# Optimization experiments

Hardware: AMD Instinct MI355X
Metric: run time of the kernel (lower is better)

## Reference

```python
import jax, jax.numpy as jnp
import numpy as np

B, L, C, H = 2, 2048, 1024, 16
D = C // H
THETA = 50000.0


def rotate_half(x):
    x1, x2 = jnp.split(x, 2, axis=-1)
    return jnp.concatenate((-x2, x1), axis=-1)


def rope_freqs(n, dim):
    inv_freq = 1.0 / (THETA ** (jnp.arange(0, dim, 2, dtype=jnp.float32) / dim))
    freqs = jnp.arange(n, dtype=jnp.float32)[:, None] * inv_freq[None, :]  # [n, dim//2]
    return jnp.concatenate((freqs, freqs), axis=-1)  # [n, dim]


def setup_inputs() -> dict:
    key = jax.random.key(0)
    ks = jax.random.split(key, 8)
    q = jax.random.normal(ks[0], (B, L, C), dtype=jnp.float32)
    mask = jax.random.randint(ks[1], (B, L), 0, 2) > 0
    mask = mask.at[:, 0].set(True)  # avoid fully-masked rows
    s = 1.0 / np.sqrt(C)
    Wq = jax.random.normal(ks[2], (C, C), dtype=jnp.float32) * s
    Wk = jax.random.normal(ks[3], (C, C), dtype=jnp.float32) * s
    Wv = jax.random.normal(ks[4], (C, C), dtype=jnp.float32) * s
    Wo = jax.random.normal(ks[5], (C, C), dtype=jnp.float32) * s
    bo = jnp.zeros((C,), dtype=jnp.float32)
    return {"q": q, "mask": mask, "Wq": Wq, "Wk": Wk, "Wv": Wv, "Wo": Wo, "bo": bo}


def reference(q, mask, Wq, Wk, Wv, Wo, bo):
    x = q
    # QKV projections (torch Linear: y = x @ W.T)
    def proj(W):
        y = jnp.einsum('blc,oc->blo', x, W)
        return y.reshape(B, L, H, D).transpose(0, 2, 1, 3)  # [B,H,L,D]
    qh, kh, vh = proj(Wq), proj(Wk), proj(Wv)
    # RoPE (L == S)
    pos = rope_freqs(L, D)  # [L, D]
    cos, sin = jnp.cos(pos), jnp.sin(pos)
    qh = qh * cos + rotate_half(qh) * sin
    kh = kh * cos + rotate_half(kh) * sin
    # masked SDPA with additive bias (-inf where mask is False)
    scale = 1.0 / np.sqrt(D)
    bias = jnp.where(mask[:, None, None, :], 0.0, -jnp.inf)  # [B,1,1,S]
    scores = jnp.einsum('bhld,bhsd->bhls', qh, kh) * scale + bias
    attn = jax.nn.softmax(scores, axis=-1)
    out = jnp.einsum('bhls,bhsd->bhld', attn, vh)
    out = out.transpose(0, 2, 1, 3).reshape(B, L, C)
    return jnp.einsum('blc,oc->blo', out, Wo) + bo
```

## Files before the change

### kernel.cpp

```cpp
#include <hip/hip_runtime.h>
#include <hip/hip_bf16.h>

typedef __hip_bfloat16 bf16;
typedef short bf16x8 __attribute__((ext_vector_type(8)));
typedef short bf16x4 __attribute__((ext_vector_type(4)));
typedef float floatx4 __attribute__((ext_vector_type(4)));

#define Bb 2
#define Ll 2048
#define Cc 1024
#define Hh 16
#define Dd 64
#define INVFREQ_LN 0.3381180763f
#define QSCALE 0.125f
#define NCONV 4096

#define GLD16(gp, lp) __builtin_amdgcn_global_load_lds( \
    (const __attribute__((address_space(1))) void*)(gp), \
    (__attribute__((address_space(3))) void*)(lp), 16, 0, 0)

__device__ inline short f2bf(float f) {
    __hip_bfloat16 h = __float2bfloat16(f);
    return *reinterpret_cast<short*>(&h);
}
__device__ inline short f2bf_rn(float f) {
    return (short)((__float_as_uint(f) + 0x8000u) >> 16);
}

__global__ __launch_bounds__(256) void convert_scan(
    const float* __restrict__ x, const float* __restrict__ wq,
    const float* __restrict__ wk, const float* __restrict__ wv,
    const float* __restrict__ wo,
    bf16* __restrict__ xb, bf16* __restrict__ wqkv, bf16* __restrict__ wob,
    const int* __restrict__ mask, int* __restrict__ cidx, int* __restrict__ valid)
{
    if (blockIdx.x >= NCONV) {
        const int b   = blockIdx.x - NCONV;
        const int tid = threadIdx.x;
        const int base = b * Ll + tid * 8;
        int m[8]; int s = 0;
        #pragma unroll
        for (int i = 0; i < 8; i++) { m[i] = mask[base + i] ? 1 : 0; s += m[i]; }
        const int lane = tid & 63;
        int xx = s;
        #pragma unroll
        for (int off = 1; off < 64; off <<= 1) {
            int y = __shfl_up(xx, off);
            if (lane >= off) xx += y;
        }
        __shared__ int wtot[4];
        if (lane == 63) wtot[tid >> 6] = xx;
        __syncthreads();
        int wbase = 0;
        const int w = tid >> 6;
        #pragma unroll
        for (int i = 0; i < 4; i++) if (i < w) wbase += wtot[i];
        int run = wbase + (xx - s);
        #pragma unroll
        for (int i = 0; i < 8; i++) { cidx[base + i] = run; run += m[i]; }
        if (tid == 255) valid[b] = run;
        return;
    }

    const int XN = (Bb * Ll * Cc) / 8;
    const int WN = (Cc * Cc) / 8;
    int i = blockIdx.x * 256 + threadIdx.x;
    const float* src; bf16* dst;
    if (i < XN)               { src = x  + (size_t)i * 8;                 dst = xb   + (size_t)i * 8; }
    else if (i < XN + WN)     { int j = i - XN;        src = wq + (size_t)j * 8; dst = wqkv + (size_t)j * 8; }
    else if (i < XN + 2*WN)   { int j = i - XN - WN;   src = wk + (size_t)j * 8; dst = wqkv + (size_t)Cc*Cc     + (size_t)j * 8; }
    else if (i < XN + 3*WN)   { int j = i - XN - 2*WN; src = wv + (size_t)j * 8; dst = wqkv + (size_t)Cc*Cc*2   + (size_t)j * 8; }
    else                      { int j = i - XN - 3*WN; src = wo + (size_t)j * 8; dst = wob  + (size_t)j * 8; }
    float4 a = *reinterpret_cast<const float4*>(src);
    float4 b = *reinterpret_cast<const float4*>(src + 4);
    float vv[8] = {a.x, a.y, a.z, a.w, b.x, b.y, b.z, b.w};
    bf16x8 o;
    #pragma unroll
    for (int t = 0; t < 8; t++) o[t] = f2bf(vv[t]);
    *reinterpret_cast<bf16x8*>(dst) = o;
}

template <int ROWS, int NTHREADS>
__device__ __forceinline__ void stage_swz(const bf16* __restrict__ g, int ldk,
                                          short* lds, int tid)
{
    #pragma unroll
    for (int s = 0; s < (ROWS * 4) / NTHREADS; s++) {
        const int idx = s * NTHREADS + tid;
        const int r   = idx >> 2;
        const int col = ((idx & 3) ^ ((r >> 1) & 3)) << 3;
        GLD16(g + (size_t)r * ldk + col, lds + idx * 8);
    }
}

#define VMCNT(N) asm volatile("s_waitcnt vmcnt(" #N ")" ::: "memory")

__global__ __launch_bounds__(512, 2) void gemm_qkv(
    const bf16* __restrict__ A, const bf16* __restrict__ W,
    bf16* __restrict__ qb, bf16* __restrict__ kb, bf16* __restrict__ vb,
    const int* __restrict__ cmask, const int* __restrict__ cidx)
{
    constexpr int K = Cc;
    constexpr int T = K / 32;

    __shared__ __align__(16) short As[3][256 * 32];
    __shared__ __align__(16) short Bs[3][256 * 32];

    const int tid  = threadIdx.x;
    const int wave = tid >> 6;
    const int lane = tid & 63;
    const int l15  = lane & 15;
    const int quad = lane >> 4;
    const int wm   = wave >> 2;
    const int wn   = wave & 3;

    const int lin = blockIdx.y * 12 + blockIdx.x;
    const int swz = (lin & 7) * 24 + (lin >> 3);
    const int m0  = (swz / 12) * 256;
    const int n0  = (swz % 12) * 256;

    const bf16* Ag = A + (size_t)m0 * K;
    const bf16* Wg = W + (size_t)n0 * K;

    const int gsw = (quad ^ ((l15 >> 1) & 3)) << 3;

    floatx4 acc[8][4];
    #pragma unroll
    for (int mt = 0; mt < 8; mt++)
        #pragma unroll
        for (int nt = 0; nt < 4; nt++)
            #pragma unroll
            for (int r = 0; r < 4; r++) acc[mt][nt][r] = 0.f;

    stage_swz<256, 512>(Ag,      K, &As[0][0], tid);
    stage_swz<256, 512>(Wg,      K, &Bs[0][0], tid);
    stage_swz<256, 512>(Ag + 32, K, &As[1][0], tid);
    stage_swz<256, 512>(Wg + 32, K, &Bs[1][0], tid);
    VMCNT(4);
    __builtin_amdgcn_s_barrier();

    int cur = 0;
    for (int t = 0; t < T; t++) {
        const short* Ac = &As[0][0] + cur * (256 * 32);
        const short* Bc = &Bs[0][0] + cur * (256 * 32);
        int nb = cur + 2; if (nb >= 3) nb -= 3;
        const int kk = (t + 2) << 5;

        bf16x8 bfr[4], af[4];
        #pragma unroll
        for (int nt = 0; nt < 4; nt++)
            bfr[nt] = *(const bf16x8*)(Bc + (wn * 64 + nt * 16 + l15) * 32 + gsw);
        #pragma unroll
        for (int mt = 0; mt < 4; mt++)
            af[mt] = *(const bf16x8*)(Ac + (wm * 128 + mt * 16 + l15) * 32 + gsw);
        if (t + 2 < T) stage_swz<256, 512>(Ag + kk, K, &As[nb][0], tid);
        __builtin_amdgcn_s_barrier();
        __builtin_amdgcn_s_setprio(1);
        #pragma unroll
        for (int mt = 0; mt < 4; mt++)
            #pragma unroll
            for (int nt = 0; nt < 4; nt++)
                acc[mt][nt] = __builtin_amdgcn_mfma_f32_16x16x32_bf16(
                    af[mt], bfr[nt], acc[mt][nt], 0, 0, 0);
        __builtin_amdgcn_s_setprio(0);
        __builtin_amdgcn_s_barrier();

        bf16x8 ag[4];
        #pragma unroll
        for (int mt = 0; mt < 4; mt++)
            ag[mt] = *(const bf16x8*)(Ac + (wm * 128 + (mt + 4) * 16 + l15) * 32 + gsw);
        if (t + 2 < T) stage_swz<256, 512>(Wg + kk, K, &Bs[nb][0], tid);
        __builtin_amdgcn_s_barrier();
        __builtin_amdgcn_s_setprio(1);
        #pragma unroll
        for (int mt = 0; mt < 4; mt++)
            #pragma unroll
            for (int nt = 0; nt < 4; nt++)
                acc[mt + 4][nt] = __builtin_amdgcn_mfma_f32_16x16x32_bf16(
                    ag[mt], bfr[nt], acc[mt + 4][nt], 0, 0, 0);
        __builtin_amdgcn_s_setprio(0);
        if (t + 2 < T) { VMCNT(4); }
        else           { VMCNT(0); }
        __builtin_amdgcn_s_barrier();

        cur++; if (cur == 3) cur = 0;
    }

    const int colbase = n0 + wn * 64;
    const int which   = colbase >> 10;
    const int hh      = (colbase & (Cc - 1)) >> 6;
    if (which == 2) {
        #pragma unroll
        for (int mt = 0; mt < 8; mt++)
            #pragma unroll
            for (int r = 0; r < 4; r++) {
                int row = m0 + wm * 128 + mt * 16 + quad * 4 + r;
                int b = row >> 11, l = row & (Ll - 1);
                if (cmask[b * Ll + l]) {
                    int c = cidx[b * Ll + l];
                    size_t head = (size_t)(b * Hh + hh) * Dd * Ll;
                    int lbase = (c & ~63) | (c & 7);
                    int lg    = (c >> 3) & 7;
                    #pragma unroll
                    for (int nt = 0; nt < 4; nt++) {
                        int d = nt * 16 + l15;
                        int pos = lbase | ((lg ^ (d & 7)) << 3);
                        vb[head + (size_t)d * Ll + pos] = __float2bfloat16(acc[mt][nt][r]);
                    }
                }
            }
    } else {
        bf16* dst = which ? kb : qb;
        const float qs = which ? 1.0f : QSCALE;
        const float base0 = __expf(-(float)l15 * INVFREQ_LN);
        const float base1 = __expf(-(float)(l15 + 16) * INVFREQ_LN);
        #pragma unroll
        for (int mt = 0; mt < 8; mt++)
            #pragma unroll
            for (int r = 0; r < 4; r++) {
                int row = m0 + wm * 128 + mt * 16 + quad * 4 + r;
                int b = row >> 11, l = row & (Ll - 1);
                int cm = 1, c = l;
                if (which == 1) {
                    cm = cmask[b * Ll + l];
                    c  = cidx[b * Ll + l];
                }
                if (cm) {
                    size_t rb = ((size_t)(b * Hh + hh) * Ll + c) * Dd;
                    #pragma unroll
                    for (int nt2 = 0; nt2 < 2; nt2++) {
                        float fr = (float)l * (nt2 ? base1 : base0);
                        float sn, cs;
                        __sincosf(fr, &sn, &cs);
                        float x1 = acc[mt][nt2][r];
                        float x2 = acc[mt][nt2 + 2][r];
                        float o1 = (x1 * cs - x2 * sn) * qs;
                        float o2 = (x2 * cs + x1 * sn) * qs;
                        int d1 = nt2 * 16 + l15;
                        int d2 = d1 + 32;
                        if (which == 1) {
                            int sw = c & 7;
                            int a1 = ((((d1 >> 3) ^ sw)) << 3) | (d1 & 7);
                            int a2 = ((((d2 >> 3) ^ sw)) << 3) | (d2 & 7);
                            dst[rb + a1] = __float2bfloat16(o1);
                            dst[rb + a2] = __float2bfloat16(o2);
                        } else {
                            dst[rb + d1] = __float2bfloat16(o1);
                            dst[rb + d2] = __float2bfloat16(o2);
                        }
                    }
                }
            }
    }
}

__global__ __launch_bounds__(256, 2) void gemm_out(
    const bf16* __restrict__ A, const bf16* __restrict__ W,
    float* __restrict__ outf, const float* __restrict__ bias)
{
    constexpr int K = Cc, N = Cc;
    constexpr int T = K / 32;

    __shared__ __align__(16) short As[3][64 * 32];
    __shared__ __align__(16) short Bs[3][128 * 32];

    const int tid  = threadIdx.x;
    const int wave = tid >> 6;
    const int lane = tid & 63;
    const int l15  = lane & 15;
    const int quad = lane >> 4;
    const int wm   = wave >> 1;
    const int wn   = wave & 1;

    const int lin = blockIdx.y * 8 + blockIdx.x;
    const int swz = (lin & 7) * 64 + (lin >> 3);
    const int m0  = (swz >> 3) * 64;
    const int n0  = (swz & 7) * 128;

    const bf16* Ag = A + (size_t)m0 * K;
    const bf16* Wg = W + (size_t)n0 * K;

    const int gsw = (quad ^ ((l15 >> 1) & 3)) << 3;

    floatx4 acc[2][4];
    #pragma unroll
    for (int mt = 0; mt < 2; mt++)
        #pragma unroll
        for (int nt = 0; nt < 4; nt++)
            #pragma unroll
            for (int r = 0; r < 4; r++) acc[mt][nt][r] = 0.f;

    stage_swz<64,  256>(Ag,      K, &As[0][0], tid);
    stage_swz<128, 256>(Wg,      K, &Bs[0][0], tid);
    stage_swz<64,  256>(Ag + 32, K, &As[1][0], tid);
    stage_swz<128, 256>(Wg + 32, K, &Bs[1][0], tid);
    VMCNT(3);
    __builtin_amdgcn_s_barrier();

    int cur = 0;
    for (int t = 0; t < T; t++) {
        const short* Ac = &As[0][0] + cur * (64 * 32);
        const short* Bc = &Bs[0][0] + cur * (128 * 32);

        if (t + 2 < T) {
            int nb = cur + 2; if (nb >= 3) nb -= 3;
            const int kk = (t + 2) << 5;
            stage_swz<64,  256>(Ag + kk, K, &As[nb][0], tid);
            stage_swz<128, 256>(Wg + kk, K, &Bs[nb][0], tid);
        }

        bf16x8 af[2], bfr[4];
        #pragma unroll
        for (int mt = 0; mt < 2; mt++)
            af[mt] = *(const bf16x8*)(Ac + (wm * 32 + mt * 16 + l15) * 32 + gsw);
        #pragma unroll
        for (int nt = 0; nt < 4; nt++)
            bfr[nt] = *(const bf16x8*)(Bc + (wn * 64 + nt * 16 + l15) * 32 + gsw);

        __builtin_amdgcn_s_setprio(1);
        #pragma unroll
        for (int mt = 0; mt < 2; mt++)
            #pragma unroll
            for (int nt = 0; nt < 4; nt++)
                acc[mt][nt] = __builtin_amdgcn_mfma_f32_16x16x32_bf16(
                    af[mt], bfr[nt], acc[mt][nt], 0, 0, 0);
        __builtin_amdgcn_s_setprio(0);

        if (t + 2 < T) { VMCNT(3); }
        else           { VMCNT(0); }
        __builtin_amdgcn_s_barrier();

        cur++; if (cur == 3) cur = 0;
    }

    #pragma unroll
    for (int mt = 0; mt < 2; mt++)
        #pragma unroll
        for (int r = 0; r < 4; r++) {
            int row = m0 + wm * 32 + mt * 16 + quad * 4 + r;
            #pragma unroll
            for (int nt = 0; nt < 4; nt++) {
                int col = n0 + wn * 64 + nt * 16 + l15;
                outf[(size_t)row * N + col] = acc[mt][nt][r] + bias[col];
            }
        }
}

#define LSTR 72

__global__ __launch_bounds__(512) void attn_mfma(
    const bf16* __restrict__ q, const bf16* __restrict__ k, const bf16* __restrict__ vt,
    const int* __restrict__ valid, bf16* __restrict__ ctx)
{
    __shared__ __align__(16) short Ks[2][64 * 64];
    __shared__ __align__(16) short Vs[2][64 * 64];
    __shared__ __align__(16) short Ps[8][16 * LSTR];

    const int tid  = threadIdx.x;
    const int wave = tid >> 6;
    const int lane = tid & 63;
    const int l15  = lane & 15;
    const int quad = lane >> 4;

    const int bh = blockIdx.x & 31;
    const int q0 = (blockIdx.x >> 5) << 7;
    const int b  = bh >> 4;
    const int h  = bh & (Hh - 1);

    const int nvalid = valid[b];
    const int ntiles = (nvalid + 63) >> 6;

    const short* qb  = (const short*)(q  + (size_t)bh * Ll * Dd);
    const short* kb  = (const short*)(k  + (size_t)bh * Ll * Dd);
    const short* vtb = (const short*)(vt + (size_t)bh * Dd * Ll);

    const int qrow = q0 + wave * 16 + l15;
    bf16x8 qa0 = *(const bf16x8*)(qb + (size_t)qrow * Dd + quad * 8);
    bf16x8 qa1 = *(const bf16x8*)(qb + (size_t)qrow * Dd + 32 + quad * 8);

    const int g0 = ((quad ^ (l15 & 7)) << 3);
    const int g1 = (((quad + 4) ^ (l15 & 7)) << 3);

    const short* vgp = vtb + (size_t)(tid >> 3) * Ll + ((tid & 7) << 3);
    short* ksl = &Ks[0][0] + tid * 8;
    short* vsl = &Vs[0][0] + tid * 8;
    const int lbuf = 64 * 64;

    floatx4 O[4];
    float l_r = 0.f;
    #pragma unroll
    for (int nt = 0; nt < 4; nt++)
        #pragma unroll
        for (int r = 0; r < 4; r++) O[nt][r] = 0.f;

    GLD16(kb + tid * 8, ksl);
    GLD16(vgp, vsl);

    for (int t = 0; t < ntiles; t++) {
        const int cur = t & 1;
        __syncthreads();
        if (t + 1 < ntiles) {
            const int s1 = (t + 1) << 6;
            GLD16(kb + (size_t)s1 * Dd + tid * 8, ksl + (cur ^ 1) * lbuf);
            GLD16(vgp + s1,                       vsl + (cur ^ 1) * lbuf);
        }

        const short* Kc = &Ks[cur][0];
        const short* Vc = &Vs[cur][0];
        floatx4 S[4];
        #pragma unroll
        for (int nt = 0; nt < 4; nt++) {
            const short* krow = Kc + (nt * 16 + l15) * 64;
            bf16x8 ka0 = *(const bf16x8*)(krow + g0);
            bf16x8 ka1 = *(const bf16x8*)(krow + g1);
            floatx4 acc; acc[0] = acc[1] = acc[2] = acc[3] = 0.f;
            acc = __builtin_amdgcn_mfma_f32_16x16x32_bf16(ka0, qa0, acc, 0, 0, 0);
            acc = __builtin_amdgcn_mfma_f32_16x16x32_bf16(ka1, qa1, acc, 0, 0, 0);
            S[nt] = acc;
        }

        if (t + 1 < ntiles) {
            #pragma unroll
            for (int nt = 0; nt < 4; nt++) {
                bf16x4 pw;
                #pragma unroll
                for (int r = 0; r < 4; r++) {
                    float p = __expf(S[nt][r]);
                    l_r += p;
                    pw[r] = f2bf_rn(p);
                }
                *(bf16x4*)&Ps[wave][l15 * LSTR + nt * 16 + quad * 4] = pw;
            }
        } else {
            const int kbase = (t << 6) + quad * 4;
            #pragma unroll
            for (int nt = 0; nt < 4; nt++) {
                bf16x4 pw;
                #pragma unroll
                for (int r = 0; r < 4; r++) {
                    float p = (kbase + nt * 16 + r < nvalid) ? __expf(S[nt][r]) : 0.f;
                    l_r += p;
                    pw[r] = f2bf_rn(p);
                }
                *(bf16x4*)&Ps[wave][l15 * LSTR + nt * 16 + quad * 4] = pw;
            }
        }

        bf16x8 pb0 = *(const bf16x8*)&Ps[wave][l15 * LSTR + quad * 8];
        bf16x8 pb1 = *(const bf16x8*)&Ps[wave][l15 * LSTR + 32 + quad * 8];
        #pragma unroll
        for (int nt = 0; nt < 4; nt++) {
            const short* vrow = Vc + (nt * 16 + l15) * 64;
            bf16x8 va0 = *(const bf16x8*)(vrow + g0);
            bf16x8 va1 = *(const bf16x8*)(vrow + g1);
            O[nt] = __builtin_amdgcn_mfma_f32_16x16x32_bf16(va0, pb0, O[nt], 0, 0, 0);
            O[nt] = __builtin_amdgcn_mfma_f32_16x16x32_bf16(va1, pb1, O[nt], 0, 0, 0);
        }
    }

    float l = l_r;
    l += __shfl_xor(l, 16);
    l += __shfl_xor(l, 32);
    const float inv = 1.0f / l;

    {
        int row = q0 + wave * 16 + l15;
        short* cp = (short*)ctx + ((size_t)(b * Ll + row)) * Cc + h * Dd;
        #pragma unroll
        for (int nt = 0; nt < 4; nt++) {
            bf16x4 ov;
            #pragma unroll
            for (int r = 0; r < 4; r++) ov[r] = f2bf_rn(O[nt][r] * inv);
            *(bf16x4*)&cp[nt * 16 + quad * 4] = ov;
        }
    }
}

extern "C" void kernel_launch(void* const* d_in, const int* in_sizes, int n_in,
                              void* d_out, int out_size, void* d_ws, size_t ws_size,
                              hipStream_t stream) {
    const float* x    = (const float*)d_in[0];
    const int*   mask = (const int*)d_in[1];
    const float* Wq   = (const float*)d_in[2];
    const float* Wk   = (const float*)d_in[3];
    const float* Wv   = (const float*)d_in[4];
    const float* Wo   = (const float*)d_in[5];
    const float* bo   = (const float*)d_in[6];
    float* out = (float*)d_out;

    const size_t per = (size_t)Bb * Hh * Ll * Dd;
    bf16* qbuf = (bf16*)d_ws;
    bf16* kbuf = qbuf + per;
    bf16* vbuf = kbuf + per;
    bf16* xb   = vbuf + per;
    bf16* wqkv = xb + per;
    bf16* wob  = wqkv + (size_t)3 * Cc * Cc;
    int*  cidx   = (int*)(wob + (size_t)Cc * Cc);
    int*  cvalid = cidx + Bb * Ll;
    bf16* ctx  = xb;

    const int M = Bb * Ll;

    convert_scan<<<NCONV + Bb, 256, 0, stream>>>(
        x, Wq, Wk, Wv, Wo, xb, wqkv, wob, mask, cidx, cvalid);

    dim3 gQKV(3 * Cc / 256, M / 256);
    gemm_qkv<<<gQKV, 512, 0, stream>>>(xb, wqkv, qbuf, kbuf, vbuf, mask, cidx);

    attn_mfma<<<Bb * Hh * (Ll / 128), 512, 0, stream>>>(qbuf, kbuf, vbuf, cvalid, ctx);

    dim3 gOut(Cc / 128, M / 64);
    gemm_out<<<gOut, 256, 0, stream>>>(ctx, wob, out, bo);
}
```

Measured before the change: 184.2 us.

## Restructure QKV GEMM pipeline with four-slot LDS ring and split B-fragment phases

The QKV projection GEMM moves from a three-slot to a four-slot LDS ring, indexed with power-of-two masks instead of a wrap-around counter. Each K-step now loads all eight A fragments up front and splits the B fragments into two halves, so each MFMA phase covers all M tiles against half the N tiles. Barriers are wrapped in compiler memory fences so LDS accesses cannot be reordered across them. The aim is cheaper slot indexing and better overlap of LDS reads with MFMA work, at the cost of more LDS per block and more live A-fragment registers.

```diff
diff --git a/kernel.cpp b/kernel.cpp
--- a/kernel.cpp
+++ b/kernel.cpp
@@ -94,6 +94,9 @@
 }
 
 #define VMCNT(N) asm volatile("s_waitcnt vmcnt(" #N ")" ::: "memory")
+#define BAR()    do { asm volatile("" ::: "memory"); \
+                      __builtin_amdgcn_s_barrier(); \
+                      asm volatile("" ::: "memory"); } while (0)
 
 __global__ __launch_bounds__(512, 2) void gemm_qkv(
     const bf16* __restrict__ A, const bf16* __restrict__ W,
@@ -102,9 +105,10 @@
 {
     constexpr int K = Cc;
     constexpr int T = K / 32;
-
-    __shared__ __align__(16) short As[3][256 * 32];
-    __shared__ __align__(16) short Bs[3][256 * 32];
+    constexpr int SL = 256 * 32;
+
+    __shared__ __align__(16) short As[4][SL];
+    __shared__ __align__(16) short Bs[4][SL];
 
     const int tid  = threadIdx.x;
     const int wave = tid >> 6;
@@ -137,53 +141,50 @@
     stage_swz<256, 512>(Ag + 32, K, &As[1][0], tid);
     stage_swz<256, 512>(Wg + 32, K, &Bs[1][0], tid);
     VMCNT(4);
-    __builtin_amdgcn_s_barrier();
-
-    int cur = 0;
+    BAR();
+
     for (int t = 0; t < T; t++) {
-        const short* Ac = &As[0][0] + cur * (256 * 32);
-        const short* Bc = &Bs[0][0] + cur * (256 * 32);
-        int nb = cur + 2; if (nb >= 3) nb -= 3;
+        const int ct = t & 3;
+        const int st = (t + 2) & 3;
+        const short* Ac = &As[ct][0];
+        const short* Bc = &Bs[ct][0];
         const int kk = (t + 2) << 5;
 
-        bf16x8 bfr[4], af[4];
-        #pragma unroll
-        for (int nt = 0; nt < 4; nt++)
+        bf16x8 af[8], bfr[4];
+        #pragma unroll
+        for (int mt = 0; mt < 8; mt++)
+            af[mt] = *(const bf16x8*)(Ac + (wm * 128 + mt * 16 + l15) * 32 + gsw);
+        #pragma unroll
+        for (int nt = 0; nt < 2; nt++)
             bfr[nt] = *(const bf16x8*)(Bc + (wn * 64 + nt * 16 + l15) * 32 + gsw);
-        #pragma unroll
-        for (int mt = 0; mt < 4; mt++)
-            af[mt] = *(const bf16x8*)(Ac + (wm * 128 + mt * 16 + l15) * 32 + gsw);
-        if (t + 2 < T) stage_swz<256, 512>(Ag + kk, K, &As[nb][0], tid);
-        __builtin_amdgcn_s_barrier();
+        if (t + 2 < T) stage_swz<256, 512>(Ag + kk, K, &As[st][0], tid);
+        BAR();
         __builtin_amdgcn_s_setprio(1);
         #pragma unroll
-        for (int mt = 0; mt < 4; mt++)
-            #pragma unroll
-            for (int nt = 0; nt < 4; nt++)
+        for (int mt = 0; mt < 8; mt++)
+            #pragma unroll
+            for (int nt = 0; nt < 2; nt++)
                 acc[mt][nt] = __builtin_amdgcn_mfma_f32_16x16x32_bf16(
                     af[mt], bfr[nt], acc[mt][nt], 0, 0, 0);
         __builtin_amdgcn_s_setprio(0);
-        __builtin_amdgcn_s_barrier();
-
-        bf16x8 ag[4];
-        #pragma unroll
-        for (int mt = 0; mt < 4; mt++)
-            ag[mt] = *(const bf16x8*)(Ac + (wm * 128 + (mt + 4) * 16 + l15) * 32 + gsw);
-        if (t + 2 < T) stage_swz<256, 512>(Wg + kk, K, &Bs[nb][0], tid);
-        __builtin_amdgcn_s_barrier();
+        BAR();
+
+        #pragma unroll
+        for (int nt = 2; nt < 4; nt++)
+            bfr[nt] = *(const bf16x8*)(Bc + (wn * 64 + nt * 16 + l15) * 32 + gsw);
+        if (t + 2 < T) stage_swz<256, 512>(Wg + kk, K, &Bs[st][0], tid);
+        BAR();
         __builtin_amdgcn_s_setprio(1);
         #pragma unroll
-        for (int mt = 0; mt < 4; mt++)
-            #pragma unroll
-            for (int nt = 0; nt < 4; nt++)
-                acc[mt + 4][nt] = __builtin_amdgcn_mfma_f32_16x16x32_bf16(
-                    ag[mt], bfr[nt], acc[mt + 4][nt], 0, 0, 0);
+        for (int mt = 0; mt < 8; mt++)
+            #pragma unroll
+            for (int nt = 2; nt < 4; nt++)
+                acc[mt][nt] = __builtin_amdgcn_mfma_f32_16x16x32_bf16(
+                    af[mt], bfr[nt], acc[mt][nt], 0, 0, 0);
         __builtin_amdgcn_s_setprio(0);
         if (t + 2 < T) { VMCNT(4); }
         else           { VMCNT(0); }
-        __builtin_amdgcn_s_barrier();
-
-        cur++; if (cur == 3) cur = 0;
+        BAR();
     }
 
     const int colbase = n0 + wn * 64;
```

Result: no change. 182.5 us (-1.0%).
